# Performance work log

Hardware: AMD Instinct MI355X
Metric: run time of the kernel (lower is better)

## Reference

```python
import jax, jax.numpy as jnp
import numpy as np

NB_POOLS = 256


def setup_inputs() -> dict:
    key = jax.random.key(0)
    x = jax.random.normal(key, (32, 32, 32, 512), dtype=jnp.float32)
    return {"x": x}


def reference(x) -> jnp.ndarray:
    B, R, C, F = x.shape
    nb_maps = R * C
    x3 = x.reshape(B, nb_maps, F)
    # self-correlation: (B, nb_maps, nb_maps), normalized by feature count
    corr = jnp.einsum('bmf,bnf->bmn', x3, x3) / F
    corr = corr.reshape(B, R, C, nb_maps)
    # percentile ranks into the descending-sorted correlation values
    ranks = jnp.round(jnp.linspace(1.0, nb_maps - 1, NB_POOLS)).astype(jnp.int32)
    # full descending sort along last axis (matches tf.nn.top_k k=nb_maps)
    x_sort = -jnp.sort(-corr, axis=-1)
    x_pool = x_sort[..., ranks]  # (B, R, C, NB_POOLS)
    return x_pool
```

## Files before the change

### kernel.cpp

```cpp
#include <hip/hip_runtime.h>


#define NMAPS 1024
#define FDIM 512
#define TM 16
#define NT 256

typedef __attribute__((ext_vector_type(8))) short short8_t;
typedef __attribute__((ext_vector_type(4))) float f32x4;
typedef _Float16 h2 __attribute__((ext_vector_type(2)));

#define SELD 0x03020504u
#define SELA 0x07060100u

__device__ __forceinline__ h2 h2min(h2 a, h2 b) { return __builtin_elementwise_min(a, b); }
__device__ __forceinline__ h2 h2max(h2 a, h2 b) { return __builtin_elementwise_max(a, b); }

__device__ __forceinline__ unsigned h2u(h2 x) { union { h2 h; unsigned u; } t; t.h = x; return t.u; }
__device__ __forceinline__ h2 u2h(unsigned x) { union { h2 h; unsigned u; } t; t.u = x; return t.h; }

__device__ __forceinline__ h2 h2swap(h2 v) {
  unsigned u = h2u(v);
  return u2h((u >> 16) | (u << 16));
}

__device__ __forceinline__ h2 h2shfl_xor(h2 v, int m) {
  union { h2 h; int i; } u;
  u.h = v;
  u.i = __shfl_xor(u.i, m, 64);
  return u.h;
}

__device__ __forceinline__ void ce_pair(h2& a, h2& b, bool d) {
  h2 mn = h2min(a, b), mx = h2max(a, b);
  a = d ? mx : mn;
  b = d ? mn : mx;
}

__device__ __forceinline__ h2 ce1(h2 w, unsigned sel) {
  h2 s = h2swap(w);
  h2 mn = h2min(w, s), mx = h2max(w, s);
#if __has_builtin(__builtin_amdgcn_perm)
  return u2h(__builtin_amdgcn_perm(h2u(mx), h2u(mn), sel));
#else
  h2 rd; rd[0] = mx[0]; rd[1] = mn[1];
  h2 ra; ra[0] = mn[0]; ra[1] = mx[1];
  return (sel == SELD) ? rd : ra;
#endif
}

__device__ __forceinline__ void intra_merge16(h2 w[8], bool d, unsigned sel) {
  ce_pair(w[0], w[4], d); ce_pair(w[1], w[5], d); ce_pair(w[2], w[6], d); ce_pair(w[3], w[7], d);
  ce_pair(w[0], w[2], d); ce_pair(w[1], w[3], d); ce_pair(w[4], w[6], d); ce_pair(w[5], w[7], d);
  ce_pair(w[0], w[1], d); ce_pair(w[2], w[3], d); ce_pair(w[4], w[5], d); ce_pair(w[6], w[7], d);
#pragma unroll
  for (int u = 0; u < 8; ++u) w[u] = ce1(w[u], sel);
}

__device__ __forceinline__ void sort16(h2 w[8], bool d, unsigned sd, unsigned si) {
  w[0] = ce1(w[0], sd); w[1] = ce1(w[1], si); w[2] = ce1(w[2], sd); w[3] = ce1(w[3], si);
  w[4] = ce1(w[4], sd); w[5] = ce1(w[5], si); w[6] = ce1(w[6], sd); w[7] = ce1(w[7], si);
  ce_pair(w[0], w[1], d); ce_pair(w[2], w[3], !d); ce_pair(w[4], w[5], d); ce_pair(w[6], w[7], !d);
  w[0] = ce1(w[0], sd); w[1] = ce1(w[1], sd); w[2] = ce1(w[2], si); w[3] = ce1(w[3], si);
  w[4] = ce1(w[4], sd); w[5] = ce1(w[5], sd); w[6] = ce1(w[6], si); w[7] = ce1(w[7], si);
  ce_pair(w[0], w[2], d); ce_pair(w[1], w[3], d); ce_pair(w[4], w[6], !d); ce_pair(w[5], w[7], !d);
  ce_pair(w[0], w[1], d); ce_pair(w[2], w[3], d); ce_pair(w[4], w[5], !d); ce_pair(w[6], w[7], !d);
  w[0] = ce1(w[0], sd); w[1] = ce1(w[1], sd); w[2] = ce1(w[2], sd); w[3] = ce1(w[3], sd);
  w[4] = ce1(w[4], si); w[5] = ce1(w[5], si); w[6] = ce1(w[6], si); w[7] = ce1(w[7], si);
  intra_merge16(w, d, sd);
}

__device__ __forceinline__ void merge32(h2 w[16], bool d) {
  const unsigned sel = d ? SELD : SELA;
#pragma unroll
  for (int u = 0; u < 8; ++u) ce_pair(w[u], w[u + 8], d);
#pragma unroll
  for (int u = 0; u < 16; ++u)
    if ((u & 4) == 0) ce_pair(w[u], w[u | 4], d);
#pragma unroll
  for (int u = 0; u < 16; ++u)
    if ((u & 2) == 0) ce_pair(w[u], w[u | 2], d);
#pragma unroll
  for (int u = 0; u < 16; ++u)
    if ((u & 1) == 0) ce_pair(w[u], w[u | 1], d);
#pragma unroll
  for (int u = 0; u < 16; ++u) w[u] = ce1(w[u], sel);
}

template<int N>
__device__ __forceinline__ void cross_ceN(h2* w, int m, bool keepmax) {
#pragma unroll
  for (int u = 0; u < N; ++u) {
    h2 p = h2shfl_xor(w[u], m);
    h2 mn = h2min(w[u], p), mx = h2max(w[u], p);
    w[u] = keepmax ? mx : mn;
  }
}
__device__ __forceinline__ void cross_ce(h2 w[8], int m, bool keepmax) {
  cross_ceN<8>(w, m, keepmax);
}

template<int K>
__device__ __forceinline__ void bitonic_stage(h2 w8[8], int lane) {
  const bool laneDesc = (K >= 16) ? ((lane & (K >> 4)) == 0) : true;
#pragma unroll
  for (int j = 512; j >= 16; j >>= 1) {
    if (j > (K >> 1)) continue;
    const int m = j >> 4;
    const bool keepmax = (((lane & m) == 0) == laneDesc);
#pragma unroll
    for (int u = 0; u < 8; ++u) {
      h2 p = h2shfl_xor(w8[u], m);
      h2 mn = h2min(w8[u], p), mx = h2max(w8[u], p);
      w8[u] = keepmax ? mx : mn;
    }
  }
#pragma unroll
  for (int j = 8; j >= 2; j >>= 1) {
    if (j > (K >> 1)) continue;
    const int jw = j >> 1;
#pragma unroll
    for (int u = 0; u < 8; ++u) {
      if ((u & jw) == 0) {
        const int v = u | jw;
        const bool desc = (K <= 8) ? (((2 * u) & K) == 0) : laneDesc;
        h2 mn = h2min(w8[u], w8[v]), mx = h2max(w8[u], w8[v]);
        w8[u] = desc ? mx : mn;
        w8[v] = desc ? mn : mx;
      }
    }
  }
#pragma unroll
  for (int u = 0; u < 8; ++u) {
    const bool desc = (K <= 8) ? (((2 * u) & K) == 0) : laneDesc;
    h2 s = h2swap(w8[u]);
    h2 mn = h2min(w8[u], s), mx = h2max(w8[u], s);
    h2 rd = (h2){mx[0], mn[1]};
    h2 ra = (h2){mn[0], mx[1]};
    w8[u] = desc ? rd : ra;
  }
}

template<int K>
__device__ __forceinline__ void bitonic_stage_tail2(h2 A[8], h2 B[8], int lane) {
  const bool laneDesc = ((lane & (K >> 4)) == 0);
#pragma unroll
  for (int j = 512; j >= 16; j >>= 1) {
    if (j > (K >> 1)) continue;
    const int m = j >> 4;
    const bool km = (((lane & m) == 0) == laneDesc);
    cross_ce(A, m, km);
    cross_ce(B, m, km);
  }
  const unsigned sel = laneDesc ? SELD : SELA;
  intra_merge16(A, laneDesc, sel);
  intra_merge16(B, laneDesc, sel);
}

__device__ __forceinline__ void run_bitonic(h2 w8[8], int lane) {
  bitonic_stage<2>(w8, lane);
  bitonic_stage<4>(w8, lane);
  bitonic_stage<8>(w8, lane);
  bitonic_stage<16>(w8, lane);
  bitonic_stage<32>(w8, lane);
  bitonic_stage<64>(w8, lane);
  bitonic_stage<128>(w8, lane);
  bitonic_stage<256>(w8, lane);
  bitonic_stage<512>(w8, lane);
  bitonic_stage<1024>(w8, lane);
}

__global__ __launch_bounds__(256) void cvt_bf16_kernel(const float* __restrict__ x,
                                                       short* __restrict__ xw, int n8) {
  int i = blockIdx.x * 256 + threadIdx.x;
  if (i >= n8) return;
  const float4* x4 = reinterpret_cast<const float4*>(x);
  float4 a = x4[i * 2], c = x4[i * 2 + 1];
  float f[8] = {a.x, a.y, a.z, a.w, c.x, c.y, c.z, c.w};
  union { short8_t v; short s[8]; } o;
#pragma unroll
  for (int j = 0; j < 8; ++j) {
    unsigned u = __float_as_uint(f[j]);
    u += 0x7fffu + ((u >> 16) & 1u);
    o.s[j] = (short)(u >> 16);
  }
  reinterpret_cast<short8_t*>(xw)[i] = o.v;
}

__global__ __launch_bounds__(512) void corr_gemm_tiled(const short* __restrict__ xw,
                                                       unsigned* __restrict__ corrW) {
  __shared__ short Asm[2][128 * 32];
  __shared__ short Bsm[2][128 * 32];
  const int tid = threadIdx.x;
  int b, tile;
  if (gridDim.x == 2048) {
    const int bid = blockIdx.x;
    const int xcd = bid & 7;
    const int j = bid >> 3;
    b = (j >> 6) * 8 + xcd;
    tile = j & 63;
  } else {
    b = blockIdx.x >> 6;
    tile = blockIdx.x & 63;
  }
  const int it = tile >> 3, jt = tile & 7;
  const int i0 = it * 128, j0 = jt * 128;
  const int lane = tid & 63;
  const int w = tid >> 6;
  const int lr = lane & 15;
  const int kg = lane >> 4;
  const short* Xb = xw + (size_t)b * NMAPS * FDIM;

  const int sr = tid >> 2;
  const int ss = (tid & 3) ^ ((sr >> 1) & 3);
  const int srcOff = sr * FDIM + ss * 8;
  const int dstOff = tid * 8;

  const int rowa = w * 16 + lr;
  const int aOff = rowa * 32 + (kg ^ ((rowa >> 1) & 3)) * 8;
  int bOff[8];
#pragma unroll
  for (int fn = 0; fn < 8; ++fn) {
    const int rowb = fn * 16 + lr;
    bOff[fn] = rowb * 32 + (kg ^ ((rowb >> 1) & 3)) * 8;
  }

  f32x4 acc[8];
#pragma unroll
  for (int fn = 0; fn < 8; ++fn) acc[fn] = (f32x4){0.f, 0.f, 0.f, 0.f};

#define STAGE(buf, kt)                                                                \
  {                                                                                   \
    const short* gA = Xb + (size_t)i0 * FDIM + srcOff + (kt) * 32;                    \
    const short* gB = Xb + (size_t)j0 * FDIM + srcOff + (kt) * 32;                    \
    __builtin_amdgcn_global_load_lds(                                                 \
        (const __attribute__((address_space(1))) unsigned*)gA,                        \
        (__attribute__((address_space(3))) unsigned*)(Asm[buf] + dstOff), 16, 0, 0);  \
    __builtin_amdgcn_global_load_lds(                                                 \
        (const __attribute__((address_space(1))) unsigned*)gB,                        \
        (__attribute__((address_space(3))) unsigned*)(Bsm[buf] + dstOff), 16, 0, 0);  \
  }

  STAGE(0, 0);
  __syncthreads();

  for (int kt = 0; kt < 16; ++kt) {
    const int cur = kt & 1;
    if (kt < 15) STAGE(cur ^ 1, kt + 1);

    short8_t a = *reinterpret_cast<const short8_t*>(Asm[cur] + aOff);
    short8_t bf[8];
#pragma unroll
    for (int fn = 0; fn < 8; ++fn)
      bf[fn] = *reinterpret_cast<const short8_t*>(Bsm[cur] + bOff[fn]);
#pragma unroll
    for (int fn = 0; fn < 8; ++fn)
      acc[fn] = __builtin_amdgcn_mfma_f32_16x16x32_bf16(bf[fn], a, acc[fn], 0, 0, 0);

    __syncthreads();
  }
#undef STAGE

  {
    const bool D128 = ((jt & 1) == 0);
    const bool d64 = ((kg & 2) == 0);
    const bool d32 = ((kg & 1) == 0);
    h2 W[16];
#pragma unroll
    for (int fn = 0; fn < 8; ++fn) {
      W[2 * fn] = (h2){(_Float16)acc[fn][0], (_Float16)acc[fn][1]};
      W[2 * fn + 1] = (h2){(_Float16)acc[fn][2], (_Float16)acc[fn][3]};
    }
    sort16(W, true, SELD, SELA);
    sort16(W + 8, false, SELA, SELD);
    merge32(W, d32);
    cross_ceN<16>(W, 16, d32 == d64);
    merge32(W, d64);
    cross_ceN<16>(W, 32, d64 == D128);
    cross_ceN<16>(W, 16, d32 == D128);
    merge32(W, D128);
    const size_t roww = ((size_t)b * NMAPS + i0 + w * 16 + lr) * 512;
    const int wq = (j0 >> 1) + kg * 16;
    union { h2 h[4]; uint4 u; } s0, s1, s2, s3;
#pragma unroll
    for (int q = 0; q < 4; ++q) { s0.h[q] = W[q]; s1.h[q] = W[4 + q]; s2.h[q] = W[8 + q]; s3.h[q] = W[12 + q]; }
    *reinterpret_cast<uint4*>(corrW + roww + wq) = s0.u;
    *reinterpret_cast<uint4*>(corrW + roww + wq + 4) = s1.u;
    *reinterpret_cast<uint4*>(corrW + roww + wq + 8) = s2.u;
    *reinterpret_cast<uint4*>(corrW + roww + wq + 12) = s3.u;
  }
}

__global__ __launch_bounds__(256) void sort_rows_kernel(const unsigned* __restrict__ corrW,
                                                        float* __restrict__ out) {
  const int tid = threadIdx.x;
  const int lane = tid & 63;
  const int rA = blockIdx.x * 8 + (tid >> 6) * 2;
  const int rB = rA + 1;
  const uint4* pa = reinterpret_cast<const uint4*>(corrW + (size_t)rA * 512);
  const uint4* pb = reinterpret_cast<const uint4*>(corrW + (size_t)rB * 512);

  h2 A[8], B[8];
  {
    union { uint4 u; h2 h[4]; } t0, t1;
    t0.u = pa[lane * 2]; t1.u = pa[lane * 2 + 1];
    A[0] = t0.h[0]; A[1] = t0.h[1]; A[2] = t0.h[2]; A[3] = t0.h[3];
    A[4] = t1.h[0]; A[5] = t1.h[1]; A[6] = t1.h[2]; A[7] = t1.h[3];
    t0.u = pb[lane * 2]; t1.u = pb[lane * 2 + 1];
    B[0] = t0.h[0]; B[1] = t0.h[1]; B[2] = t0.h[2]; B[3] = t0.h[3];
    B[4] = t1.h[0]; B[5] = t1.h[1]; B[6] = t1.h[2]; B[7] = t1.h[3];
  }

  bitonic_stage_tail2<256>(A, B, lane);
  bitonic_stage_tail2<512>(A, B, lane);
  bitonic_stage_tail2<1024>(A, B, lane);

  float* oa = out + (size_t)rA * 256;
  float* ob = out + (size_t)rB * 256;
#pragma unroll
  for (int u = 0; u < 8; ++u) {
#pragma unroll
    for (int hh = 0; hh < 2; ++hh) {
      const int i = lane * 16 + 2 * u + hh;
      const int p = (int)rint((double)(i - 1) * (255.0 / 1022.0));
      const int rk = (int)rint(1.0 + (double)p * (1022.0 / 255.0));
      if (rk == i) {
        oa[p] = (float)A[u][hh] * (1.f / FDIM);
        ob[p] = (float)B[u][hh] * (1.f / FDIM);
      }
    }
  }
}

__global__ __launch_bounds__(NT) void selfcorr_mfma_kernel(const short* __restrict__ xw,
                                                           float* __restrict__ out) {
  __shared__ alignas(16) h2 SH[TM * 512];
  const int tid = threadIdx.x;
  const int b = blockIdx.y;
  const int m0 = blockIdx.x * TM;
  const int lane = tid & 63;
  const int wid = tid >> 6;
  const int lr = lane & 15;
  const int kg = lane >> 4;
  const int wc = wid * 256;
  const short* Xb = xw + (size_t)b * NMAPS * FDIM;

  f32x4 acc[16];
#pragma unroll
  for (int t = 0; t < 16; ++t) acc[t] = (f32x4){0.f, 0.f, 0.f, 0.f};

  for (int kk = 0; kk < 16; ++kk) {
    const short8_t* base = reinterpret_cast<const short8_t*>(Xb + kk * 32 + kg * 8);
    short8_t afrag = base[(size_t)(m0 + lr) * 64];
    short8_t bfrag[16];
#pragma unroll
    for (int t = 0; t < 16; ++t) bfrag[t] = base[(size_t)(wc + t * 16 + lr) * 64];
#pragma unroll
    for (int t = 0; t < 16; ++t)
      acc[t] = __builtin_amdgcn_mfma_f32_16x16x32_bf16(bfrag[t], afrag, acc[t], 0, 0, 0);
  }

  {
    const int xorv = (lr & 7) << 2;
#pragma unroll
    for (int t = 0; t < 16; ++t) {
      h2 lo = (h2){(_Float16)(acc[t][0] * (1.f / FDIM)), (_Float16)(acc[t][1] * (1.f / FDIM))};
      h2 hi = (h2){(_Float16)(acc[t][2] * (1.f / FDIM)), (_Float16)(acc[t][3] * (1.f / FDIM))};
      const int W = (wc >> 1) + t * 8 + kg * 2;
      const int phys = lr * 512 + (W ^ xorv);
      union { h2 h[2]; uint2 u; } pk;
      pk.h[0] = lo; pk.h[1] = hi;
      *reinterpret_cast<uint2*>(&SH[phys]) = pk.u;
    }
  }
  __syncthreads();

  const int rowbase = wid * 4;
  for (int rr = rowbase; rr < rowbase + 4; ++rr) {
    const int rx = (rr & 7) << 2;
    h2 w8[8];
#pragma unroll
    for (int q = 0; q < 2; ++q) {
      const int p4 = rr * 512 + ((lane * 8 + q * 4) ^ rx);
      union { uint4 u; h2 h[4]; } un;
      un.u = *reinterpret_cast<const uint4*>(&SH[p4]);
      w8[q * 4 + 0] = un.h[0]; w8[q * 4 + 1] = un.h[1];
      w8[q * 4 + 2] = un.h[2]; w8[q * 4 + 3] = un.h[3];
    }
    run_bitonic(w8, lane);
#pragma unroll
    for (int q = 0; q < 2; ++q) {
      const int p4 = rr * 512 + ((lane * 8 + q * 4) ^ rx);
      union { uint4 u; h2 h[4]; } un;
      un.h[0] = w8[q * 4 + 0]; un.h[1] = w8[q * 4 + 1];
      un.h[2] = w8[q * 4 + 2]; un.h[3] = w8[q * 4 + 3];
      *reinterpret_cast<uint4*>(&SH[p4]) = un.u;
    }
  }
  __builtin_amdgcn_wave_barrier();

#pragma unroll
  for (int i = 0; i < 16; ++i) {
    const int rr = rowbase + (i >> 2);
    const int p = lane + ((i & 3) << 6);
    const int rank = (int)rint(1.0 + (double)p * (1022.0 / 255.0));
    const int Wr = (rank >> 1) ^ ((rr & 7) << 2);
    h2 hv = SH[rr * 512 + Wr];
    out[((size_t)(b * NMAPS + m0 + rr) << 8) + p] = (float)hv[rank & 1];
  }
}

__device__ __forceinline__ int sw4(int row, int c4) {
  return (row << 8) | (c4 ^ ((c4 >> 3) & 7));
}
__device__ __forceinline__ void ce(float& a, float& b, bool desc) {
  float mn = fminf(a, b);
  float mx = fmaxf(a, b);
  a = desc ? mx : mn;
  b = desc ? mn : mx;
}

__global__ __launch_bounds__(NT) void selfcorr_pool_kernel(const float* __restrict__ x,
                                                           float* __restrict__ out) {
  __shared__ float lds[TM * NMAPS];
  float4* S4 = reinterpret_cast<float4*>(lds);
  const int tid = threadIdx.x;
  const int b = blockIdx.y;
  const int m0 = blockIdx.x * TM;
  const float4* Xb = reinterpret_cast<const float4*>(x) + (size_t)b * NMAPS * (FDIM / 4);

  float4* A4 = reinterpret_cast<float4*>(lds);
#pragma unroll
  for (int idx = tid; idx < TM * (FDIM / 4); idx += NT) {
    A4[idx] = Xb[(m0 + (idx >> 7)) * 128 + (idx & 127)];
  }
  __syncthreads();

  float acc[TM][4];
#pragma unroll
  for (int m = 0; m < TM; ++m)
#pragma unroll
    for (int j = 0; j < 4; ++j) acc[m][j] = 0.0f;

  float4 nb0 = Xb[(tid + 0) * 128];
  float4 nb1 = Xb[(tid + 256) * 128];
  float4 nb2 = Xb[(tid + 512) * 128];
  float4 nb3 = Xb[(tid + 768) * 128];
  for (int k4 = 0; k4 < 128; ++k4) {
    float4 b0 = nb0, b1 = nb1, b2 = nb2, b3 = nb3;
    const int kn = (k4 < 127) ? (k4 + 1) : 127;
    nb0 = Xb[(tid + 0) * 128 + kn];
    nb1 = Xb[(tid + 256) * 128 + kn];
    nb2 = Xb[(tid + 512) * 128 + kn];
    nb3 = Xb[(tid + 768) * 128 + kn];
#pragma unroll
    for (int m = 0; m < TM; ++m) {
      float4 a = A4[m * 128 + k4];
      acc[m][0] += a.x * b0.x + a.y * b0.y + a.z * b0.z + a.w * b0.w;
      acc[m][1] += a.x * b1.x + a.y * b1.y + a.z * b1.z + a.w * b1.w;
      acc[m][2] += a.x * b2.x + a.y * b2.y + a.z * b2.z + a.w * b2.w;
      acc[m][3] += a.x * b3.x + a.y * b3.y + a.z * b3.z + a.w * b3.w;
    }
  }
  __syncthreads();

#pragma unroll
  for (int m = 0; m < TM; ++m) {
#pragma unroll
    for (int j = 0; j < 4; ++j) {
      const int n = tid + (j << 8);
      lds[sw4(m, n >> 2) * 4 + (n & 3)] = acc[m][j] * (1.0f / FDIM);
    }
  }
  __syncthreads();

#pragma unroll
  for (int c = 0; c < 2; ++c) {
    const int cid = tid + (c << 8);
    const int row = cid >> 5;
    const int chunk = cid & 31;
    float r[32];
#pragma unroll
    for (int q = 0; q < 8; ++q) {
      float4 t = S4[sw4(row, (chunk << 3) + q)];
      r[q * 4 + 0] = t.x; r[q * 4 + 1] = t.y; r[q * 4 + 2] = t.z; r[q * 4 + 3] = t.w;
    }
    const bool D = ((chunk & 1) == 0);
#pragma unroll
    for (int k2 = 2; k2 <= 32; k2 <<= 1) {
#pragma unroll
      for (int j = k2 >> 1; j > 0; j >>= 1) {
#pragma unroll
        for (int i = 0; i < 32; ++i) {
          if ((i & j) == 0) ce(r[i], r[i | j], ((i & k2) == 0) ? D : !D);
        }
      }
    }
#pragma unroll
    for (int q = 0; q < 8; ++q) {
      S4[sw4(row, (chunk << 3) + q)] =
          make_float4(r[q * 4 + 0], r[q * 4 + 1], r[q * 4 + 2], r[q * 4 + 3]);
    }
  }
  __syncthreads();

  for (int k = 64; k <= NMAPS; k <<= 1) {
    for (int j = k >> 1; j >= 32; j >>= 1) {
      const int j4 = j >> 2;
      const int kq = k >> 2;
#pragma unroll
      for (int q = 0; q < 8; ++q) {
        const int g = tid + (q << 8);
        const int row = g >> 7;
        const int v = g & 127;
        const int i4 = ((v & ~(j4 - 1)) << 1) | (v & (j4 - 1));
        const bool desc = ((i4 & kq) == 0);
        const int ia = sw4(row, i4);
        const int ib = sw4(row, i4 + j4);
        float4 va = S4[ia];
        float4 vb = S4[ib];
        float4 lo, hi;
        lo.x = fminf(va.x, vb.x); hi.x = fmaxf(va.x, vb.x);
        lo.y = fminf(va.y, vb.y); hi.y = fmaxf(va.y, vb.y);
        lo.z = fminf(va.z, vb.z); hi.z = fmaxf(va.z, vb.z);
        lo.w = fminf(va.w, vb.w); hi.w = fmaxf(va.w, vb.w);
        S4[ia] = desc ? hi : lo;
        S4[ib] = desc ? lo : hi;
      }
      __syncthreads();
    }
#pragma unroll
    for (int c = 0; c < 2; ++c) {
      const int cid = tid + (c << 8);
      const int row = cid >> 5;
      const int chunk = cid & 31;
      const bool D = (((chunk << 5) & k) == 0);
      float r[32];
#pragma unroll
      for (int q = 0; q < 8; ++q) {
        float4 t = S4[sw4(row, (chunk << 3) + q)];
        r[q * 4 + 0] = t.x; r[q * 4 + 1] = t.y; r[q * 4 + 2] = t.z; r[q * 4 + 3] = t.w;
      }
#pragma unroll
      for (int j = 16; j > 0; j >>= 1) {
#pragma unroll
        for (int i = 0; i < 32; ++i) {
          if ((i & j) == 0) ce(r[i], r[i | j], D);
        }
      }
#pragma unroll
      for (int q = 0; q < 8; ++q) {
        S4[sw4(row, (chunk << 3) + q)] =
            make_float4(r[q * 4 + 0], r[q * 4 + 1], r[q * 4 + 2], r[q * 4 + 3]);
      }
    }
    __syncthreads();
  }

  const int p = tid;
  const int rank = (int)rint(1.0 + (double)p * (1022.0 / 255.0));
#pragma unroll
  for (int m = 0; m < TM; ++m) {
    out[((size_t)(b * NMAPS + m0 + m) << 8) + p] = lds[sw4(m, rank >> 2) * 4 + (rank & 3)];
  }
}

extern "C" void kernel_launch(void* const* d_in, const int* in_sizes, int n_in,
                              void* d_out, int out_size, void* d_ws, size_t ws_size,
                              hipStream_t stream) {
  const float* x = reinterpret_cast<const float*>(d_in[0]);
  float* out = reinterpret_cast<float*>(d_out);
  const int nelem = in_sizes[0];
  const int B = nelem / (NMAPS * FDIM);
  const size_t need_split = (size_t)nelem * 2 + (size_t)B * NMAPS * NMAPS * 2;
  if (ws_size >= need_split) {
    short* xw = reinterpret_cast<short*>(d_ws);
    unsigned* corrW = reinterpret_cast<unsigned*>((char*)d_ws + (size_t)nelem * 2);
    const int n8 = nelem / 8;
    hipLaunchKernelGGL(cvt_bf16_kernel, dim3((n8 + 255) / 256), dim3(256), 0, stream, x, xw, n8);
    hipLaunchKernelGGL(corr_gemm_tiled, dim3(64 * B), dim3(512), 0, stream, xw, corrW);
    hipLaunchKernelGGL(sort_rows_kernel, dim3(B * NMAPS / 8), dim3(256), 0, stream, corrW, out);
  } else if (ws_size >= (size_t)nelem * 2) {
    short* xw = reinterpret_cast<short*>(d_ws);
    const int n8 = nelem / 8;
    hipLaunchKernelGGL(cvt_bf16_kernel, dim3((n8 + 255) / 256), dim3(256), 0, stream, x, xw, n8);
    hipLaunchKernelGGL(selfcorr_mfma_kernel, dim3(NMAPS / TM, B), dim3(NT), 0, stream, xw, out);
  } else {
    hipLaunchKernelGGL(selfcorr_pool_kernel, dim3(NMAPS / TM, B), dim3(NT), 0, stream, x, out);
  }
}
```

Before: 161.2 us.

## Enlarge GEMM block tile to 256x128 so each B fragment feeds two MFMAs

Each block of the correlation GEMM now computes a 256x128 output tile instead of 128x128, loading two A sub-tiles per k-step and reusing each B fragment for two MFMA calls. The grid halves to 32 blocks per batch, with the XCD-aware block mapping adjusted to match. This cuts global and LDS traffic for B per output element and improves the MFMA-to-load ratio. In exchange it doubles accumulator registers, increases LDS use, and launches fewer blocks (1024), which may lower occupancy and load balance.

```diff
diff --git a/kernel.cpp b/kernel.cpp
--- a/kernel.cpp
+++ b/kernel.cpp
@@ -189,22 +189,22 @@
 
 __global__ __launch_bounds__(512) void corr_gemm_tiled(const short* __restrict__ xw,
                                                        unsigned* __restrict__ corrW) {
-  __shared__ short Asm[2][128 * 32];
+  __shared__ short Asm[2][2][128 * 32];
   __shared__ short Bsm[2][128 * 32];
   const int tid = threadIdx.x;
   int b, tile;
-  if (gridDim.x == 2048) {
+  if (gridDim.x == 1024) {
     const int bid = blockIdx.x;
     const int xcd = bid & 7;
     const int j = bid >> 3;
-    b = (j >> 6) * 8 + xcd;
-    tile = j & 63;
+    b = (j >> 5) * 8 + xcd;
+    tile = j & 31;
   } else {
-    b = blockIdx.x >> 6;
-    tile = blockIdx.x & 63;
-  }
-  const int it = tile >> 3, jt = tile & 7;
-  const int i0 = it * 128, j0 = jt * 128;
+    b = blockIdx.x >> 5;
+    tile = blockIdx.x & 31;
+  }
+  const int it2 = tile >> 3, jt = tile & 7;
+  const int i0 = it2 * 256, j0 = jt * 128;
   const int lane = tid & 63;
   const int w = tid >> 6;
   const int lr = lane & 15;
@@ -225,17 +225,26 @@
     bOff[fn] = rowb * 32 + (kg ^ ((rowb >> 1) & 3)) * 8;
   }
 
-  f32x4 acc[8];
-#pragma unroll
-  for (int fn = 0; fn < 8; ++fn) acc[fn] = (f32x4){0.f, 0.f, 0.f, 0.f};
+  f32x4 acc0[8], acc1[8];
+#pragma unroll
+  for (int fn = 0; fn < 8; ++fn) {
+    acc0[fn] = (f32x4){0.f, 0.f, 0.f, 0.f};
+    acc1[fn] = (f32x4){0.f, 0.f, 0.f, 0.f};
+  }
 
 #define STAGE(buf, kt)                                                                \
   {                                                                                   \
-    const short* gA = Xb + (size_t)i0 * FDIM + srcOff + (kt) * 32;                    \
+    const short* gA0 = Xb + (size_t)i0 * FDIM + srcOff + (kt) * 32;                   \
+    const short* gA1 = Xb + (size_t)(i0 + 128) * FDIM + srcOff + (kt) * 32;           \
     const short* gB = Xb + (size_t)j0 * FDIM + srcOff + (kt) * 32;                    \
     __builtin_amdgcn_global_load_lds(                                                 \
-        (const __attribute__((address_space(1))) unsigned*)gA,                        \
-        (__attribute__((address_space(3))) unsigned*)(Asm[buf] + dstOff), 16, 0, 0);  \
+        (const __attribute__((address_space(1))) unsigned*)gA0,                       \
+        (__attribute__((address_space(3))) unsigned*)(Asm[buf][0] + dstOff), 16, 0,   \
+        0);                                                                           \
+    __builtin_amdgcn_global_load_lds(                                                 \
+        (const __attribute__((address_space(1))) unsigned*)gA1,                       \
+        (__attribute__((address_space(3))) unsigned*)(Asm[buf][1] + dstOff), 16, 0,   \
+        0);                                                                           \
     __builtin_amdgcn_global_load_lds(                                                 \
         (const __attribute__((address_space(1))) unsigned*)gB,                        \
         (__attribute__((address_space(3))) unsigned*)(Bsm[buf] + dstOff), 16, 0, 0);  \
@@ -248,23 +257,28 @@
     const int cur = kt & 1;
     if (kt < 15) STAGE(cur ^ 1, kt + 1);
 
-    short8_t a = *reinterpret_cast<const short8_t*>(Asm[cur] + aOff);
+    short8_t a0 = *reinterpret_cast<const short8_t*>(Asm[cur][0] + aOff);
+    short8_t a1 = *reinterpret_cast<const short8_t*>(Asm[cur][1] + aOff);
     short8_t bf[8];
 #pragma unroll
     for (int fn = 0; fn < 8; ++fn)
       bf[fn] = *reinterpret_cast<const short8_t*>(Bsm[cur] + bOff[fn]);
 #pragma unroll
-    for (int fn = 0; fn < 8; ++fn)
-      acc[fn] = __builtin_amdgcn_mfma_f32_16x16x32_bf16(bf[fn], a, acc[fn], 0, 0, 0);
+    for (int fn = 0; fn < 8; ++fn) {
+      acc0[fn] = __builtin_amdgcn_mfma_f32_16x16x32_bf16(bf[fn], a0, acc0[fn], 0, 0, 0);
+      acc1[fn] = __builtin_amdgcn_mfma_f32_16x16x32_bf16(bf[fn], a1, acc1[fn], 0, 0, 0);
+    }
 
     __syncthreads();
   }
 #undef STAGE
 
-  {
-    const bool D128 = ((jt & 1) == 0);
-    const bool d64 = ((kg & 2) == 0);
-    const bool d32 = ((kg & 1) == 0);
+  const bool D128 = ((jt & 1) == 0);
+  const bool d64 = ((kg & 2) == 0);
+  const bool d32 = ((kg & 1) == 0);
+#pragma unroll
+  for (int t2 = 0; t2 < 2; ++t2) {
+    const f32x4* acc = (t2 == 0) ? acc0 : acc1;
     h2 W[16];
 #pragma unroll
     for (int fn = 0; fn < 8; ++fn) {
@@ -279,7 +293,7 @@
     cross_ceN<16>(W, 32, d64 == D128);
     cross_ceN<16>(W, 16, d32 == D128);
     merge32(W, D128);
-    const size_t roww = ((size_t)b * NMAPS + i0 + w * 16 + lr) * 512;
+    const size_t roww = ((size_t)b * NMAPS + i0 + t2 * 128 + w * 16 + lr) * 512;
     const int wq = (j0 >> 1) + kg * 16;
     union { h2 h[4]; uint4 u; } s0, s1, s2, s3;
 #pragma unroll
@@ -578,7 +592,7 @@
     unsigned* corrW = reinterpret_cast<unsigned*>((char*)d_ws + (size_t)nelem * 2);
     const int n8 = nelem / 8;
     hipLaunchKernelGGL(cvt_bf16_kernel, dim3((n8 + 255) / 256), dim3(256), 0, stream, x, xw, n8);
-    hipLaunchKernelGGL(corr_gemm_tiled, dim3(64 * B), dim3(512), 0, stream, xw, corrW);
+    hipLaunchKernelGGL(corr_gemm_tiled, dim3(32 * B), dim3(512), 0, stream, xw, corrW);
     hipLaunchKernelGGL(sort_rows_kernel, dim3(B * NMAPS / 8), dim3(256), 0, stream, corrW, out);
   } else if (ws_size >= (size_t)nelem * 2) {
     short* xw = reinterpret_cast<short*>(d_ws);
```

After: 163.6 us. No clear change (+1.5%).
